# Performance work log

Measured on AMD Instinct MI355X. Metric: run time of the kernel, lower is better.

Reference implementation:

```python
import jax, jax.numpy as jnp
import numpy as np

B, T, N, K = 8, 256, 128, 64
EPS = 1e-12  # torch.nn.functional.normalize clamp


def setup_inputs() -> dict:
    key = jax.random.key(0)
    ks = jax.random.split(key, 6)
    observation = jax.random.normal(ks[0], (B, T, K), dtype=jnp.float32)
    duration = jax.random.randint(ks[1], (B,), 1, T + 1)  # in [1, T]
    # time-varying transition matrices, strictly positive (probabilities pre-normalization)
    transition = jax.random.uniform(ks[2], (T, B, N, N), dtype=jnp.float32, minval=0.05, maxval=1.0)
    start_prob = jax.random.uniform(ks[3], (B, N), dtype=jnp.float32, minval=0.05, maxval=1.0)
    W_emit = jax.random.normal(ks[4], (K, N), dtype=jnp.float32) * 0.05
    b_emit = jnp.zeros((N,), dtype=jnp.float32)
    return {"observation": observation, "duration": duration, "transition": transition,
            "start_prob": start_prob, "W_emit": W_emit, "b_emit": b_emit}


def _log_emission(observation, W_emit, b_emit):
    # emission module: linear K->N then log-softmax over states -> [B,T,N]
    logits = jnp.einsum('btk,kn->btn', observation, W_emit) + b_emit
    return jax.nn.log_softmax(logits, axis=-1)


def reference(observation, duration, transition, start_prob, W_emit, b_emit):
    log_emit = _log_emission(observation, W_emit, b_emit)            # [B,T,N]
    # L1-normalize transitions along target dim (dim=2 of [B,N,N]) then log
    l1 = jnp.clip(jnp.sum(jnp.abs(transition), axis=-1, keepdims=True), EPS)
    logT = jnp.log(transition / l1)                                  # [T,B,N,N]

    la0 = log_emit[:, 0, :] + jnp.log(start_prob)                    # [B,N]

    def step(la_prev, xs):
        le_t, lT_t = xs                                              # [B,N], [B,N,N]
        # log-domain matmul: out[b,j] = logsumexp_k la_prev[b,k] + logT[b,k,j]
        la = le_t + jax.nn.logsumexp(la_prev[:, :, None] + lT_t, axis=1)
        return la, la

    le_seq = jnp.swapaxes(log_emit, 0, 1)                            # [T,B,N]
    _, alphas = jax.lax.scan(step, la0, (le_seq[1:], logT[1:]))      # [T-1,B,N]
    log_alpha = jnp.concatenate([la0[:, None, :], jnp.swapaxes(alphas, 0, 1)], axis=1)  # [B,T,N]

    log_sums = jax.nn.logsumexp(log_alpha, axis=2)                   # [B,T]
    log_probs = jnp.take_along_axis(log_sums, (duration - 1)[:, None], axis=1)  # [B,1]
    return log_probs
```

## Files before the change

kernel.cpp:

```cpp
#include <hip/hip_runtime.h>
#include <math.h>
#include <stdint.h>

#define B_ 8
#define T_ 256
#define N_ 128
#define K_ 64
#define NCH 32
#define LOG128 4.852030263919617f
#define STRIDE_S 4128

typedef __attribute__((ext_vector_type(2))) unsigned int u32x2;
typedef __attribute__((ext_vector_type(4))) unsigned int u32x4;
typedef __attribute__((ext_vector_type(4))) float f32x4;
typedef __attribute__((ext_vector_type(8))) short short8;

__device__ __forceinline__ uint32_t cvtpk(float lo, float hi) {
    uint32_t r;
    asm("v_cvt_pk_bf16_f32 %0, %1, %2" : "=v"(r) : "v"(lo), "v"(hi));
    return r;
}
__device__ __forceinline__ float blo(uint32_t w) { return __uint_as_float(w << 16); }
__device__ __forceinline__ float bhi(uint32_t w) { return __uint_as_float(w & 0xffff0000u); }

#define TRRD(dst, addr) asm volatile("ds_read_b64_tr_b16 %0, %1" : "=v"(dst) : "v"(addr) : "memory")
#define WAITL8  { asm volatile("s_waitcnt lgkmcnt(8)"  ::: "memory"); __builtin_amdgcn_sched_barrier(0); }
#define WAITL0  { asm volatile("s_waitcnt lgkmcnt(0)"  ::: "memory"); __builtin_amdgcn_sched_barrier(0); }
#define BARRIER_LG() { asm volatile("s_waitcnt lgkmcnt(0)" ::: "memory"); \
                       __builtin_amdgcn_s_barrier(); \
                       __builtin_amdgcn_sched_barrier(0); }

__global__ __launch_bounds__(128) void k_emit(
    const float* __restrict__ obs,
    const int*   __restrict__ dur,
    const float* __restrict__ W,
    const float* __restrict__ bias,
    float* __restrict__ e)
{
    int bt = blockIdx.x;
    int b  = bt >> 8;
    int t  = bt & 255;
    if (t >= dur[b]) return;
    int n = threadIdx.x;
    __shared__ float o[K_];
    __shared__ float wmax[2];
    __shared__ float wsum[2];
    if (n < K_) o[n] = obs[(size_t)bt * K_ + n];
    __syncthreads();
    float acc = bias[n];
    #pragma unroll
    for (int k = 0; k < K_; ++k)
        acc = fmaf(o[k], W[k * N_ + n], acc);
    float m = acc;
    #pragma unroll
    for (int off = 32; off; off >>= 1) m = fmaxf(m, __shfl_xor(m, off));
    int w = n >> 6;
    if ((n & 63) == 0) wmax[w] = m;
    __syncthreads();
    float M = fmaxf(wmax[0], wmax[1]);
    float ex = expf(acc - M);
    float s = ex;
    #pragma unroll
    for (int off = 32; off; off >>= 1) s += __shfl_xor(s, off);
    if ((n & 63) == 0) wsum[w] = s;
    __syncthreads();
    float S = wsum[0] + wsum[1];
    e[(size_t)bt * N_ + n] = ex / S;
}

__global__ __launch_bounds__(512, 1) void k_chunk(
    const float* __restrict__ trans,
    const int*   __restrict__ dur,
    const float* __restrict__ e,
    uint32_t* __restrict__ gout)
{
    const int bc = blockIdx.x;
    const int b  = bc & 7;
    const int c  = bc >> 3;
    const int d  = dur[b];
    const int t0 = c * 8 + 1;
    if (t0 > d - 1) return;
    int te = c * 8 + 8; if (te > d - 1) te = d - 1;

    const int tid  = threadIdx.x;
    const int lane = tid & 63;
    const int wv   = tid >> 6;
    const int cc   = lane & 15;
    const int gq   = lane >> 4;

    __shared__ __align__(16) uint8_t ldsC[2][8 * STRIDE_S];
    __shared__ __align__(16) uint8_t strips[8 * STRIDE_S];

    {
        uint32_t* sw = (uint32_t*)(strips + wv * STRIDE_S);
        #pragma unroll
        for (int i = 0; i < 16; ++i) sw[lane + i * 64] = 0;
        if (lane < 16)
            ((uint16_t*)(strips + wv * STRIDE_S))[(16 * wv + lane) * 16 + lane] = 0x3F80u;
    }

    const uint32_t sbase = (uint32_t)(uintptr_t)&strips[wv * STRIDE_S];
    const uint32_t lt    = (uint32_t)(cc * 2 + gq * 256);
    const int row0 = tid >> 5;
    const int jbp  = (tid & 31) >> 2;
    const int cc0  = (tid & 3) << 2;

    f32x4 acc[8];

    float4 v[8];
    float  ev[8];
    {
        const float4* gp = (const float4*)(trans + (((size_t)t0 * B_ + b) << 14));
        #pragma unroll
        for (int i = 0; i < 8; ++i) v[i] = gp[tid + i * 512];
        #pragma unroll
        for (int i = 0; i < 8; ++i)
            ev[i] = e[((size_t)b * T_ + (t0 - 1)) * N_ + row0 + i * 16];
    }

    int buf = 0;
    for (int t = t0; t <= te; ++t, buf ^= 1) {
        uint8_t* cb = ldsC[buf];
        const uint32_t cbase = (uint32_t)(uintptr_t)cb;

        #pragma unroll
        for (int i = 0; i < 8; ++i) {
            float ps = (v[i].x + v[i].y) + (v[i].z + v[i].w);
            ps += __shfl_xor(ps, 1);
            ps += __shfl_xor(ps, 2);
            ps += __shfl_xor(ps, 4);
            ps += __shfl_xor(ps, 8);
            ps += __shfl_xor(ps, 16);
            float sc = 128.0f * ev[i] / ps;
            uint32_t p0 = cvtpk(v[i].x * sc, v[i].y * sc);
            uint32_t p1 = cvtpk(v[i].z * sc, v[i].w * sc);
            *(uint2*)(cb + jbp * STRIDE_S + (row0 + i * 16) * 32 + cc0 * 2) = make_uint2(p0, p1);
        }

        if (t < te) {
            const float4* gp = (const float4*)(trans + (((size_t)(t + 1) * B_ + b) << 14));
            #pragma unroll
            for (int i = 0; i < 8; ++i) v[i] = gp[tid + i * 512];
            #pragma unroll
            for (int i = 0; i < 8; ++i)
                ev[i] = e[((size_t)b * T_ + t) * N_ + row0 + i * 16];
        }
        BARRIER_LG();

        u32x2 ra[8];
        #pragma unroll
        for (int kb = 0; kb < 4; ++kb) {
            uint32_t ad = sbase + (uint32_t)(kb * 1024) + lt;
            TRRD(ra[2 * kb],     ad);
            TRRD(ra[2 * kb + 1], ad + 128);
        }
        u32x2 rb[2][8];
#define ISSUE_B(S, JB) { \
        _Pragma("unroll") \
        for (int kb = 0; kb < 4; ++kb) { \
            uint32_t bd = cbase + (uint32_t)((JB) * STRIDE_S + kb * 1024) + lt; \
            TRRD(rb[S][2 * kb],     bd); \
            TRRD(rb[S][2 * kb + 1], bd + 128); } }
#define MFMA_JB(JB, S) { \
        f32x4 d4 = (f32x4){0.f, 0.f, 0.f, 0.f}; \
        _Pragma("unroll") \
        for (int kb = 0; kb < 4; ++kb) { \
            u32x4 tmp = (u32x4){rb[S][2 * kb].x, rb[S][2 * kb].y, rb[S][2 * kb + 1].x, rb[S][2 * kb + 1].y}; \
            short8 Bf = __builtin_bit_cast(short8, tmp); \
            d4 = __builtin_amdgcn_mfma_f32_16x16x32_bf16(A[kb], Bf, d4, 0, 0, 0); } \
        acc[JB] = d4; }

        ISSUE_B(0, 0);
        ISSUE_B(1, 1);
        WAITL8;
        short8 A[4];
        #pragma unroll
        for (int kb = 0; kb < 4; ++kb) {
            u32x4 tmp = (u32x4){ra[2 * kb].x, ra[2 * kb].y, ra[2 * kb + 1].x, ra[2 * kb + 1].y};
            A[kb] = __builtin_bit_cast(short8, tmp);
        }
        MFMA_JB(0, 0);
        ISSUE_B(0, 2); WAITL8; MFMA_JB(1, 1);
        ISSUE_B(1, 3); WAITL8; MFMA_JB(2, 0);
        ISSUE_B(0, 4); WAITL8; MFMA_JB(3, 1);
        ISSUE_B(1, 5); WAITL8; MFMA_JB(4, 0);
        ISSUE_B(0, 6); WAITL8; MFMA_JB(5, 1);
        ISSUE_B(1, 7); WAITL8; MFMA_JB(6, 0);
        WAITL0;                MFMA_JB(7, 1);
#undef ISSUE_B
#undef MFMA_JB

        #pragma unroll
        for (int jb = 0; jb < 8; ++jb) {
            uint32_t p0 = cvtpk(acc[jb][0], acc[jb][1]);
            uint32_t p1 = cvtpk(acc[jb][2], acc[jb][3]);
            *(uint2*)(strips + wv * STRIDE_S + (jb * 16 + cc) * 32 + gq * 8) = make_uint2(p0, p1);
        }
    }

    uint32_t* gdst = gout + ((size_t)(b * NCH + c) << 13);
    #pragma unroll
    for (int kb = 0; kb < 4; ++kb) {
        u32x2 e0, e1;
        uint32_t ad = sbase + (uint32_t)(kb * 1024) + lt;
        TRRD(e0, ad);
        TRRD(e1, ad + 128);
        WAITL0;
        u32x4 o = (u32x4){e0.x, e0.y, e1.x, e1.y};
        *(u32x4*)(gdst + (size_t)((16 * wv + cc) * 64 + kb * 16 + gq * 4)) = o;
    }
}

__global__ __launch_bounds__(256, 1) void k_comb(
    const uint32_t* __restrict__ gtiles,
    const int*   __restrict__ dur,
    const float* __restrict__ sp,
    const float* __restrict__ e,
    float* __restrict__ out)
{
    const int b   = blockIdx.x;
    const int tid = threadIdx.x;
    const int wv  = tid >> 6;
    const int l   = tid & 63;
    const int d   = dur[b];
    const int nc  = (d - 1 + 7) >> 3;

    __shared__ float  gl[2][N_];
    __shared__ float2 part[2][4][64];

    float g0 = sp[b * N_ + 2 * l];
    float g1 = sp[b * N_ + 2 * l + 1];
    float S  = -(float)(d - 1) * LOG128;
    *(float2*)&gl[0][2 * l] = make_float2(g0, g1);

    const uint32_t* gb = gtiles + (((size_t)b * NCH) << 13) + l;
    uint32_t cwA[32], cwB[32], cwC[32];
    int p = 0;

#define LOADCH(P, C) { \
    const uint32_t* gp_ = gb + ((size_t)(C) << 13); \
    _Pragma("unroll") \
    for (int kk = 0; kk < 32; ++kk) P[kk] = gp_[(size_t)(wv * 32 + kk) * 64]; }

#define CSTEP(CUR, NXT, CIDX) { \
    if ((CIDX) + 2 < nc) LOADCH(NXT, (CIDX) + 2); \
    float n0a = 0.f, n0b = 0.f, n1a = 0.f, n1b = 0.f; \
    _Pragma("unroll") \
    for (int kk = 0; kk < 32; kk += 2) { \
        float gk0 = gl[p][wv * 32 + kk]; \
        float gk1 = gl[p][wv * 32 + kk + 1]; \
        n0a = fmaf(blo(CUR[kk]),     gk0, n0a); \
        n1a = fmaf(bhi(CUR[kk]),     gk0, n1a); \
        n0b = fmaf(blo(CUR[kk + 1]), gk1, n0b); \
        n1b = fmaf(bhi(CUR[kk + 1]), gk1, n1b); } \
    part[p][wv][l] = make_float2(n0a + n0b, n1a + n1b); \
    BARRIER_LG(); \
    float2 q0 = part[p][0][l], q1 = part[p][1][l], q2 = part[p][2][l], q3 = part[p][3][l]; \
    float s0 = (q0.x + q1.x) + (q2.x + q3.x); \
    float s1 = (q0.y + q1.y) + (q2.y + q3.y); \
    float mx = fmaxf(s0, s1); \
    _Pragma("unroll") \
    for (int of = 1; of < 64; of <<= 1) mx = fmaxf(mx, __shfl_xor(mx, of)); \
    float mr = __builtin_amdgcn_rcpf(mx); \
    g0 = s0 * mr; g1 = s1 * mr; \
    S -= __logf(mr); \
    *(float2*)&gl[p ^ 1][2 * l] = make_float2(g0, g1); \
    p ^= 1; \
}

    if (nc > 0) {
        LOADCH(cwA, 0);
        if (nc > 1) LOADCH(cwB, 1);
        int c = 0;
        while (true) {
            CSTEP(cwA, cwC, c); ++c; if (c >= nc) break;
            CSTEP(cwB, cwA, c); ++c; if (c >= nc) break;
            CSTEP(cwC, cwB, c); ++c; if (c >= nc) break;
        }
    }
#undef LOADCH
#undef CSTEP

    float e0 = e[((size_t)b * T_ + (d - 1)) * N_ + 2 * l];
    float e1 = e[((size_t)b * T_ + (d - 1)) * N_ + 2 * l + 1];
    float sv = g0 * e0 + g1 * e1;
    #pragma unroll
    for (int of = 1; of < 64; of <<= 1) sv += __shfl_xor(sv, of);
    if (tid == 0) out[b] = S + logf(sv);
}

extern "C" void kernel_launch(void* const* d_in, const int* in_sizes, int n_in,
                              void* d_out, int out_size, void* d_ws, size_t ws_size,
                              hipStream_t stream) {
    const float* obs   = (const float*)d_in[0];
    const int*   dur   = (const int*)  d_in[1];
    const float* trans = (const float*)d_in[2];
    const float* sp    = (const float*)d_in[3];
    const float* W     = (const float*)d_in[4];
    const float* bias  = (const float*)d_in[5];
    float* out = (float*)d_out;

    float* e = (float*)d_ws;
    uint32_t* gout = (uint32_t*)((char*)d_ws + (size_t)B_ * T_ * N_ * 4);

    hipLaunchKernelGGL(k_emit,  dim3(B_ * T_),  dim3(128), 0, stream, obs, dur, W, bias, e);
    hipLaunchKernelGGL(k_chunk, dim3(B_ * NCH), dim3(512), 0, stream, trans, dur, e, gout);
    hipLaunchKernelGGL(k_comb,  dim3(B_),       dim3(256), 0, stream, gout, dur, sp, e, out);
}
```

Measured before the change: 69.08 us.

## Deepen prefetch pipelines in chunk-matmul and combine kernels

After: 67.59 us. -2.1%, faster.

```diff
diff --git a/kernel.cpp b/kernel.cpp
--- a/kernel.cpp
+++ b/kernel.cpp
@@ -105,56 +105,27 @@
     const int jbp  = (tid & 31) >> 2;
     const int cc0  = (tid & 3) << 2;
 
-    f32x4 acc[8];
-
-    float4 v[8];
-    float  ev[8];
+    float4 vA[8], vB[8];
+    float  eA[8], eB[8];
     {
         const float4* gp = (const float4*)(trans + (((size_t)t0 * B_ + b) << 14));
         #pragma unroll
-        for (int i = 0; i < 8; ++i) v[i] = gp[tid + i * 512];
+        for (int i = 0; i < 8; ++i) vA[i] = gp[tid + i * 512];
         #pragma unroll
         for (int i = 0; i < 8; ++i)
-            ev[i] = e[((size_t)b * T_ + (t0 - 1)) * N_ + row0 + i * 16];
+            eA[i] = e[((size_t)b * T_ + (t0 - 1)) * N_ + row0 + i * 16];
+    }
+    if (t0 + 1 <= te) {
+        const float4* gp = (const float4*)(trans + (((size_t)(t0 + 1) * B_ + b) << 14));
+        #pragma unroll
+        for (int i = 0; i < 8; ++i) vB[i] = gp[tid + i * 512];
+        #pragma unroll
+        for (int i = 0; i < 8; ++i)
+            eB[i] = e[((size_t)b * T_ + t0) * N_ + row0 + i * 16];
     }
 
     int buf = 0;
-    for (int t = t0; t <= te; ++t, buf ^= 1) {
-        uint8_t* cb = ldsC[buf];
-        const uint32_t cbase = (uint32_t)(uintptr_t)cb;
-
-        #pragma unroll
-        for (int i = 0; i < 8; ++i) {
-            float ps = (v[i].x + v[i].y) + (v[i].z + v[i].w);
-            ps += __shfl_xor(ps, 1);
-            ps += __shfl_xor(ps, 2);
-            ps += __shfl_xor(ps, 4);
-            ps += __shfl_xor(ps, 8);
-            ps += __shfl_xor(ps, 16);
-            float sc = 128.0f * ev[i] / ps;
-            uint32_t p0 = cvtpk(v[i].x * sc, v[i].y * sc);
-            uint32_t p1 = cvtpk(v[i].z * sc, v[i].w * sc);
-            *(uint2*)(cb + jbp * STRIDE_S + (row0 + i * 16) * 32 + cc0 * 2) = make_uint2(p0, p1);
-        }
-
-        if (t < te) {
-            const float4* gp = (const float4*)(trans + (((size_t)(t + 1) * B_ + b) << 14));
-            #pragma unroll
-            for (int i = 0; i < 8; ++i) v[i] = gp[tid + i * 512];
-            #pragma unroll
-            for (int i = 0; i < 8; ++i)
-                ev[i] = e[((size_t)b * T_ + t) * N_ + row0 + i * 16];
-        }
-        BARRIER_LG();
-
-        u32x2 ra[8];
-        #pragma unroll
-        for (int kb = 0; kb < 4; ++kb) {
-            uint32_t ad = sbase + (uint32_t)(kb * 1024) + lt;
-            TRRD(ra[2 * kb],     ad);
-            TRRD(ra[2 * kb + 1], ad + 128);
-        }
-        u32x2 rb[2][8];
+
 #define ISSUE_B(S, JB) { \
         _Pragma("unroll") \
         for (int kb = 0; kb < 4; ++kb) { \
@@ -170,33 +141,80 @@
             d4 = __builtin_amdgcn_mfma_f32_16x16x32_bf16(A[kb], Bf, d4, 0, 0, 0); } \
         acc[JB] = d4; }
 
-        ISSUE_B(0, 0);
-        ISSUE_B(1, 1);
-        WAITL8;
-        short8 A[4];
-        #pragma unroll
-        for (int kb = 0; kb < 4; ++kb) {
-            u32x4 tmp = (u32x4){ra[2 * kb].x, ra[2 * kb].y, ra[2 * kb + 1].x, ra[2 * kb + 1].y};
-            A[kb] = __builtin_bit_cast(short8, tmp);
-        }
-        MFMA_JB(0, 0);
-        ISSUE_B(0, 2); WAITL8; MFMA_JB(1, 1);
-        ISSUE_B(1, 3); WAITL8; MFMA_JB(2, 0);
-        ISSUE_B(0, 4); WAITL8; MFMA_JB(3, 1);
-        ISSUE_B(1, 5); WAITL8; MFMA_JB(4, 0);
-        ISSUE_B(0, 6); WAITL8; MFMA_JB(5, 1);
-        ISSUE_B(1, 7); WAITL8; MFMA_JB(6, 0);
-        WAITL0;                MFMA_JB(7, 1);
+#define STEP(VC, EC) { \
+    uint8_t* cb = ldsC[buf]; \
+    const uint32_t cbase = (uint32_t)(uintptr_t)cb; \
+     \
+    _Pragma("unroll") \
+    for (int i = 0; i < 8; ++i) { \
+        float ps = (VC[i].x + VC[i].y) + (VC[i].z + VC[i].w); \
+        ps += __shfl_xor(ps, 1); \
+        ps += __shfl_xor(ps, 2); \
+        ps += __shfl_xor(ps, 4); \
+        ps += __shfl_xor(ps, 8); \
+        ps += __shfl_xor(ps, 16); \
+        float sc = 128.0f * EC[i] * __builtin_amdgcn_rcpf(ps); \
+        uint32_t p0 = cvtpk(VC[i].x * sc, VC[i].y * sc); \
+        uint32_t p1 = cvtpk(VC[i].z * sc, VC[i].w * sc); \
+        *(uint2*)(cb + jbp * STRIDE_S + (row0 + i * 16) * 32 + cc0 * 2) = make_uint2(p0, p1); \
+    } \
+     \
+    if (t + 2 <= te) { \
+        const float4* gp = (const float4*)(trans + (((size_t)(t + 2) * B_ + b) << 14)); \
+        _Pragma("unroll") \
+        for (int i = 0; i < 8; ++i) VC[i] = gp[tid + i * 512]; \
+        _Pragma("unroll") \
+        for (int i = 0; i < 8; ++i) \
+            EC[i] = e[((size_t)b * T_ + (t + 1)) * N_ + row0 + i * 16]; \
+    } \
+    BARRIER_LG(); \
+     \
+    { \
+        u32x2 ra[8]; \
+        _Pragma("unroll") \
+        for (int kb = 0; kb < 4; ++kb) { \
+            uint32_t ad = sbase + (uint32_t)(kb * 1024) + lt; \
+            TRRD(ra[2 * kb],     ad); \
+            TRRD(ra[2 * kb + 1], ad + 128); \
+        } \
+        u32x2 rb[2][8]; \
+        f32x4 acc[8]; \
+        ISSUE_B(0, 0); \
+        ISSUE_B(1, 1); \
+        WAITL8; \
+        short8 A[4]; \
+        _Pragma("unroll") \
+        for (int kb = 0; kb < 4; ++kb) { \
+            u32x4 tmp = (u32x4){ra[2 * kb].x, ra[2 * kb].y, ra[2 * kb + 1].x, ra[2 * kb + 1].y}; \
+            A[kb] = __builtin_bit_cast(short8, tmp); \
+        } \
+        MFMA_JB(0, 0); \
+        ISSUE_B(0, 2); WAITL8; MFMA_JB(1, 1); \
+        ISSUE_B(1, 3); WAITL8; MFMA_JB(2, 0); \
+        ISSUE_B(0, 4); WAITL8; MFMA_JB(3, 1); \
+        ISSUE_B(1, 5); WAITL8; MFMA_JB(4, 0); \
+        ISSUE_B(0, 6); WAITL8; MFMA_JB(5, 1); \
+        ISSUE_B(1, 7); WAITL8; MFMA_JB(6, 0); \
+        WAITL0;                MFMA_JB(7, 1); \
+         \
+        _Pragma("unroll") \
+        for (int jb = 0; jb < 8; ++jb) { \
+            uint32_t p0 = cvtpk(acc[jb][0], acc[jb][1]); \
+            uint32_t p1 = cvtpk(acc[jb][2], acc[jb][3]); \
+            *(uint2*)(strips + wv * STRIDE_S + (jb * 16 + cc) * 32 + gq * 8) = make_uint2(p0, p1); \
+        } \
+    } \
+    buf ^= 1; \
+}
+
+    int t = t0;
+    while (true) {
+        STEP(vA, eA); ++t; if (t > te) break;
+        STEP(vB, eB); ++t; if (t > te) break;
+    }
+#undef STEP
 #undef ISSUE_B
 #undef MFMA_JB
-
-        #pragma unroll
-        for (int jb = 0; jb < 8; ++jb) {
-            uint32_t p0 = cvtpk(acc[jb][0], acc[jb][1]);
-            uint32_t p1 = cvtpk(acc[jb][2], acc[jb][3]);
-            *(uint2*)(strips + wv * STRIDE_S + (jb * 16 + cc) * 32 + gq * 8) = make_uint2(p0, p1);
-        }
-    }
 
     uint32_t* gdst = gout + ((size_t)(b * NCH + c) << 13);
     #pragma unroll
@@ -234,7 +252,7 @@
     *(float2*)&gl[0][2 * l] = make_float2(g0, g1);
 
     const uint32_t* gb = gtiles + (((size_t)b * NCH) << 13) + l;
-    uint32_t cwA[32], cwB[32], cwC[32];
+    uint32_t cwA[32], cwB[32], cwC[32], cwD[32];
     int p = 0;
 
 #define LOADCH(P, C) { \
@@ -243,7 +261,7 @@
     for (int kk = 0; kk < 32; ++kk) P[kk] = gp_[(size_t)(wv * 32 + kk) * 64]; }
 
 #define CSTEP(CUR, NXT, CIDX) { \
-    if ((CIDX) + 2 < nc) LOADCH(NXT, (CIDX) + 2); \
+    if ((CIDX) + 3 < nc) LOADCH(NXT, (CIDX) + 3); \
     float n0a = 0.f, n0b = 0.f, n1a = 0.f, n1b = 0.f; \
     _Pragma("unroll") \
     for (int kk = 0; kk < 32; kk += 2) { \
@@ -271,11 +289,13 @@
     if (nc > 0) {
         LOADCH(cwA, 0);
         if (nc > 1) LOADCH(cwB, 1);
+        if (nc > 2) LOADCH(cwC, 2);
         int c = 0;
         while (true) {
-            CSTEP(cwA, cwC, c); ++c; if (c >= nc) break;
+            CSTEP(cwA, cwD, c); ++c; if (c >= nc) break;
             CSTEP(cwB, cwA, c); ++c; if (c >= nc) break;
             CSTEP(cwC, cwB, c); ++c; if (c >= nc) break;
+            CSTEP(cwD, cwC, c); ++c; if (c >= nc) break;
         }
     }
 #undef LOADCH
```
